# Performance work log

Hardware: AMD Instinct MI355X
Metric: run time of the kernel (lower is better)

## Reference

```python
import jax, jax.numpy as jnp
import numpy as np


def setup_inputs() -> dict:
    key = jax.random.key(0)
    ks = jax.random.split(key, 7)
    B, D, T, H = 32, 512, 4096, 512
    return {
        "query": jax.random.normal(ks[0], (B, D, 1), dtype=jnp.float32),
        "keys": jax.random.normal(ks[1], (B, D, T), dtype=jnp.float32),
        "values": jax.random.normal(ks[2], (B, D, T), dtype=jnp.float32),
        "w42": 0.01 * jax.random.normal(ks[3], (H, 2 * D), dtype=jnp.float32),
        "b4": 0.01 * jax.random.normal(ks[4], (H, 1), dtype=jnp.float32),
        "w54": 0.01 * jax.random.normal(ks[5], (1, H), dtype=jnp.float32),
        "b5": 0.01 * jax.random.normal(ks[6], (1, 1), dtype=jnp.float32),
    }


def reference(query, keys, values, w42, b4, w54, b5):
    D = keys.shape[1]
    # cat([keys, query.repeat T], dim=1) then w42 @ cat ==
    # w42[:, :D] @ keys + w42[:, D:] @ query (broadcast over T)
    n4 = (jnp.einsum('hd,bdt->bht', w42[:, :D], keys)
          + jnp.einsum('hd,bdo->bho', w42[:, D:], query)  # [B,H,1], broadcasts over T
          + b4)                                            # [H,1] broadcasts
    a4 = jnp.tanh(n4)                                      # [B,H,T]
    n5 = jnp.einsum('oh,bht->bot', w54, a4) + b5           # [B,1,T]
    # transpose(1,2) -> [B,T,1], softmax over dim=1 (T)
    a5 = jax.nn.softmax(n5[:, 0, :], axis=-1)              # [B,T]
    a6 = jnp.einsum('bvt,bt->bv', values, a5)[..., None]   # [B,Dv,1]
    return a6
```

## Files before the change

kernel.cpp:

```cpp
#include <hip/hip_runtime.h>
#include <hip/hip_bf16.h>
#include <cstdint>
#include <cstddef>

typedef __attribute__((ext_vector_type(4))) float f32x4;
typedef __attribute__((ext_vector_type(8))) short s16x8;
typedef __attribute__((ext_vector_type(4))) unsigned short u16x4;
typedef __attribute__((ext_vector_type(8))) unsigned short u16x8;

#define NB 32
#define DD 512
#define TT 4096
#define HH 512
#define TB 64
#define BK 32
#define NKK 16

__device__ __forceinline__ unsigned short f2bf(float f) {
  uint32_t u = __builtin_bit_cast(uint32_t, f);
  u += 0x7fffu + ((u >> 16) & 1u);
  return (unsigned short)(u >> 16);
}

__device__ __forceinline__ float tanh_fast(float x) {
  x = fminf(fmaxf(x, -15.f), 15.f);
  float e = __expf(2.f * x);
  return (e - 1.f) / (e + 1.f);
}

__global__ void kConvT(const float* __restrict__ w42, u16x8* __restrict__ W1swz) {
  int g = blockIdx.x * 256 + threadIdx.x;
  int h = g & 511, sk = g >> 9;
  int kk = sk >> 2, s = sk & 3;
  const float* src = &w42[h * 1024 + kk * 32 + s * 8];
  f32x4 v0 = *reinterpret_cast<const f32x4*>(src);
  f32x4 v1 = *reinterpret_cast<const f32x4*>(src + 4);
  u16x8 c;
  c[0] = f2bf(v0.x); c[1] = f2bf(v0.y); c[2] = f2bf(v0.z); c[3] = f2bf(v0.w);
  c[4] = f2bf(v1.x); c[5] = f2bf(v1.y); c[6] = f2bf(v1.z); c[7] = f2bf(v1.w);
  W1swz[kk * 2048 + s * 512 + h] = c;
}

__global__ void kQterm(const float* __restrict__ w42, const float* __restrict__ query,
                       const float* __restrict__ b4, float* __restrict__ qterm) {
  int wid = blockIdx.x * 4 + (threadIdx.x >> 6);
  int lane = threadIdx.x & 63;
  int b = wid >> 9, h = wid & 511;
  const float* wr = &w42[h * 1024 + 512];
  const float* q  = &query[b * 512];
  int d = lane * 8;
  f32x4 w0 = *(const f32x4*)&wr[d], w1 = *(const f32x4*)&wr[d + 4];
  f32x4 q0 = *(const f32x4*)&q[d],  q1 = *(const f32x4*)&q[d + 4];
  float s = w0.x*q0.x + w0.y*q0.y + w0.z*q0.z + w0.w*q0.w
          + w1.x*q1.x + w1.y*q1.y + w1.z*q1.z + w1.w*q1.w;
  #pragma unroll
  for (int off = 32; off; off >>= 1) s += __shfl_xor(s, off);
  if (lane == 0) qterm[b * 512 + h] = s + b4[h];
}

__global__ __launch_bounds__(256, 2) void kGemmE(
    const float* __restrict__ keys, const u16x8* __restrict__ W1swz,
    const float* __restrict__ qterm, const float* __restrict__ w54,
    float* __restrict__ e, float* __restrict__ Zp) {
  __shared__ s16x8 Bs[2 * 4 * 64];
  __shared__ float red[4][64];

  int bid = blockIdx.x;
  int b = bid >> 6, tblk = bid & 63;
  int t0 = tblk * TB;
  int tid = threadIdx.x, lane = tid & 63, w = tid >> 6;
  int lr = lane & 15, lg = lane >> 4;

  const float* kp = keys + (size_t)b * DD * TT + (size_t)(w * 8) * TT + t0 + lane;
  const s16x8* ap = reinterpret_cast<const s16x8*>(W1swz) + lg * 512 + w * 128 + lr;

  f32x4 acc[8][4];
  #pragma unroll
  for (int m = 0; m < 8; ++m)
    #pragma unroll
    for (int n = 0; n < 4; ++n) acc[m][n] = (f32x4){0.f, 0.f, 0.f, 0.f};

  s16x8 af[2][8];
  float r[2][8];
  #pragma unroll
  for (int m = 0; m < 8; ++m) af[0][m] = ap[m * 16];
  #pragma unroll
  for (int j = 0; j < 8; ++j) r[0][j] = kp[(size_t)j * TT];
  #pragma unroll
  for (int j = 0; j < 8; ++j) r[1][j] = kp[(size_t)(BK + j) * TT];

  #pragma unroll
  for (int kk = 0; kk < NKK; ++kk) {
    const int cur = kk & 1;
    s16x8 c;
    #pragma unroll
    for (int j = 0; j < 8; ++j) c[j] = (short)f2bf(r[cur][j]);
    Bs[(cur * 4 + w) * 64 + lane] = c;

    if (kk + 1 < NKK) {
      #pragma unroll
      for (int m = 0; m < 8; ++m) af[cur ^ 1][m] = ap[(kk + 1) * 2048 + m * 16];
    }
    if (kk + 2 < NKK) {
      const float* kp2 = kp + (size_t)(kk + 2) * BK * TT;
      #pragma unroll
      for (int j = 0; j < 8; ++j) r[cur][j] = kp2[(size_t)j * TT];
    }

    asm volatile("s_waitcnt lgkmcnt(0)" ::: "memory");
    __builtin_amdgcn_s_barrier();

    s16x8 bf[4];
    #pragma unroll
    for (int n = 0; n < 4; ++n)
      bf[n] = Bs[(cur * 4 + lg) * 64 + n * 16 + lr];

    #pragma unroll
    for (int m = 0; m < 8; ++m)
      #pragma unroll
      for (int n = 0; n < 4; ++n)
        acc[m][n] = __builtin_amdgcn_mfma_f32_16x16x32_bf16(af[cur][m], bf[n], acc[m][n], 0, 0, 0);
  }

  float part[4] = {0.f, 0.f, 0.f, 0.f};
  int hb = w * 128;
  #pragma unroll
  for (int m = 0; m < 8; ++m) {
    #pragma unroll
    for (int rr = 0; rr < 4; ++rr) {
      int h = hb + m * 16 + lg * 4 + rr;
      float qv = qterm[b * HH + h];
      float wv = w54[h];
      #pragma unroll
      for (int n = 0; n < 4; ++n)
        part[n] += wv * tanh_fast(acc[m][n][rr] + qv);
    }
  }
  #pragma unroll
  for (int n = 0; n < 4; ++n) {
    part[n] += __shfl_xor(part[n], 16);
    part[n] += __shfl_xor(part[n], 32);
  }
  if (lane < 16) {
    #pragma unroll
    for (int n = 0; n < 4; ++n) red[w][n * 16 + lane] = part[n];
  }
  __syncthreads();
  if (tid < 64) {
    float v = red[0][tid] + red[1][tid] + red[2][tid] + red[3][tid];
    float ev = __expf(v);
    e[b * TT + t0 + tid] = ev;
    float z = ev;
    #pragma unroll
    for (int off = 32; off; off >>= 1) z += __shfl_xor(z, off);
    if (tid == 0) Zp[b * 64 + tblk] = z;
  }
}

__global__ void kZinv(const float* __restrict__ Zp, float* __restrict__ Zinv) {
  int b = blockIdx.x, lane = threadIdx.x;
  float z = Zp[b * 64 + lane];
  #pragma unroll
  for (int off = 32; off; off >>= 1) z += __shfl_xor(z, off);
  if (lane == 0) Zinv[b] = 1.f / z;
}

__global__ void kOut(const float* __restrict__ values, const float* __restrict__ e,
                     const float* __restrict__ Zinv, float* __restrict__ out) {
  int blk = blockIdx.x;
  int b = blk >> 7;
  int wid = threadIdx.x >> 6, lane = threadIdx.x & 63;
  int v = (blk & 127) * 4 + wid;
  const float* row = &values[((size_t)b * 512 + v) * TT];
  const float* wv = &e[b * TT];
  float s = 0.f;
  #pragma unroll
  for (int i = 0; i < 16; ++i) {
    int t = (i * 64 + lane) * 4;
    f32x4 x = *(const f32x4*)&row[t];
    f32x4 y = *(const f32x4*)&wv[t];
    s += x.x * y.x + x.y * y.y + x.z * y.z + x.w * y.w;
  }
  #pragma unroll
  for (int off = 32; off; off >>= 1) s += __shfl_xor(s, off);
  if (lane == 0) out[b * 512 + v] = s * Zinv[b];
}

extern "C" void kernel_launch(void* const* d_in, const int* in_sizes, int n_in,
                              void* d_out, int out_size, void* d_ws, size_t ws_size,
                              hipStream_t stream) {
  const float* query  = (const float*)d_in[0];
  const float* keys   = (const float*)d_in[1];
  const float* values = (const float*)d_in[2];
  const float* w42    = (const float*)d_in[3];
  const float* b4     = (const float*)d_in[4];
  const float* w54    = (const float*)d_in[5];
  float* out = (float*)d_out;

  char* ws = (char*)d_ws;
  u16x8* W1swz = (u16x8*)ws;
  float* qterm = (float*)(ws + (512 << 10));
  float* Zp    = (float*)(ws + (576 << 10));
  float* Zinv  = (float*)(ws + (592 << 10));
  float* e     = (float*)(ws + (640 << 10));

  kConvT <<<128, 256, 0, stream>>>(w42, W1swz);
  kQterm <<<4096, 256, 0, stream>>>(w42, query, b4, qterm);
  kGemmE <<<2048, 256, 0, stream>>>(keys, W1swz, qterm, w54, e, Zp);
  kZinv  <<<32, 64, 0, stream>>>(Zp, Zinv);
  kOut   <<<4096, 256, 0, stream>>>(values, e, Zinv, out);
}
```

Before: 172.4 us.

## Retile GEMM over H quarters and 128-wide T tiles with swizzled LDS

The score GEMM now tiles each block over 128 hidden units and 128 time steps instead of all 512 hidden units by 64 steps. Blocks are remapped with a grid swizzle so the four H-quarter blocks for the same keys tile run close together and share keys in cache. Partial scores per H quarter go to a buffer, and a new softmax kernel sums them, exponentiates and computes the normalizer. Other changes: LDS XOR swizzling, packed bf16 conversion instructions, occupancy raised to 3, and nontemporal values loads with split accumulators in the output kernel. The cost is the extra partial-score traffic and keys re-reads across H blocks.

```diff
diff --git a/kernel.cpp b/kernel.cpp
--- a/kernel.cpp
+++ b/kernel.cpp
@@ -5,21 +5,24 @@
 
 typedef __attribute__((ext_vector_type(4))) float f32x4;
 typedef __attribute__((ext_vector_type(8))) short s16x8;
-typedef __attribute__((ext_vector_type(4))) unsigned short u16x4;
 typedef __attribute__((ext_vector_type(8))) unsigned short u16x8;
 
 #define NB 32
 #define DD 512
 #define TT 4096
 #define HH 512
-#define TB 64
-#define BK 32
 #define NKK 16
 
 __device__ __forceinline__ unsigned short f2bf(float f) {
   uint32_t u = __builtin_bit_cast(uint32_t, f);
   u += 0x7fffu + ((u >> 16) & 1u);
   return (unsigned short)(u >> 16);
+}
+
+__device__ __forceinline__ uint32_t cvtpk(float a, float b) {
+  uint32_t d;
+  asm("v_cvt_pk_bf16_f32 %0, %1, %2" : "=v"(d) : "v"(a), "v"(b));
+  return d;
 }
 
 __device__ __forceinline__ float tanh_fast(float x) {
@@ -58,53 +61,67 @@
   if (lane == 0) qterm[b * 512 + h] = s + b4[h];
 }
 
-__global__ __launch_bounds__(256, 2) void kGemmE(
+__global__ __launch_bounds__(256, 3) void kGemmE(
     const float* __restrict__ keys, const u16x8* __restrict__ W1swz,
     const float* __restrict__ qterm, const float* __restrict__ w54,
-    float* __restrict__ e, float* __restrict__ Zp) {
-  __shared__ s16x8 Bs[2 * 4 * 64];
-  __shared__ float red[4][64];
-
-  int bid = blockIdx.x;
-  int b = bid >> 6, tblk = bid & 63;
-  int t0 = tblk * TB;
-  int tid = threadIdx.x, lane = tid & 63, w = tid >> 6;
+    float* __restrict__ n5p) {
+  __shared__ s16x8 Bs[2][512];
+  __shared__ float red[2][128];
+
+  int p = blockIdx.x;
+  int lix = (p & 7) * 512 + (p >> 3);
+  int hq = lix & 3, tt = (lix >> 2) & 31, b = lix >> 7;
+  int h0 = hq * 128, t0 = tt * 128;
+
+  int tid = threadIdx.x, lane = tid & 63, wid = tid >> 6;
+  int wh = wid & 1, wt = wid >> 1;
   int lr = lane & 15, lg = lane >> 4;
 
-  const float* kp = keys + (size_t)b * DD * TT + (size_t)(w * 8) * TT + t0 + lane;
-  const s16x8* ap = reinterpret_cast<const s16x8*>(W1swz) + lg * 512 + w * 128 + lr;
-
-  f32x4 acc[8][4];
-  #pragma unroll
-  for (int m = 0; m < 8; ++m)
+  int s = tid >> 6, ta = tid & 63;
+  const float* kp = keys + (size_t)b * DD * TT + (size_t)(s * 8) * TT + t0 + ta;
+  int wiA = s * 128 + (ta ^ s), wiB = s * 128 + ((ta + 64) ^ s);
+  const s16x8* ap = reinterpret_cast<const s16x8*>(W1swz) + lg * 512 + h0 + wh * 64 + lr;
+  int rci[4];
+  #pragma unroll
+  for (int n = 0; n < 4; ++n) {
+    int t = wt * 64 + n * 16 + lr;
+    rci[n] = lg * 128 + (t ^ lg);
+  }
+
+  f32x4 acc[4][4];
+  #pragma unroll
+  for (int m = 0; m < 4; ++m)
     #pragma unroll
     for (int n = 0; n < 4; ++n) acc[m][n] = (f32x4){0.f, 0.f, 0.f, 0.f};
 
-  s16x8 af[2][8];
-  float r[2][8];
-  #pragma unroll
-  for (int m = 0; m < 8; ++m) af[0][m] = ap[m * 16];
-  #pragma unroll
-  for (int j = 0; j < 8; ++j) r[0][j] = kp[(size_t)j * TT];
-  #pragma unroll
-  for (int j = 0; j < 8; ++j) r[1][j] = kp[(size_t)(BK + j) * TT];
+  float r[16];
+  #pragma unroll
+  for (int j = 0; j < 8; ++j) r[j] = kp[(size_t)j * TT];
+  #pragma unroll
+  for (int j = 0; j < 8; ++j) r[8 + j] = kp[(size_t)j * TT + 64];
 
   #pragma unroll
   for (int kk = 0; kk < NKK; ++kk) {
     const int cur = kk & 1;
-    s16x8 c;
-    #pragma unroll
-    for (int j = 0; j < 8; ++j) c[j] = (short)f2bf(r[cur][j]);
-    Bs[(cur * 4 + w) * 64 + lane] = c;
+    s16x8 af[4];
+    #pragma unroll
+    for (int m = 0; m < 4; ++m) af[m] = ap[kk * 2048 + m * 16];
+
+    union { uint32_t u[4]; s16x8 v; } ca, cb;
+    #pragma unroll
+    for (int j = 0; j < 4; ++j) {
+      ca.u[j] = cvtpk(r[2 * j], r[2 * j + 1]);
+      cb.u[j] = cvtpk(r[8 + 2 * j], r[9 + 2 * j]);
+    }
+    Bs[cur][wiA] = ca.v;
+    Bs[cur][wiB] = cb.v;
 
     if (kk + 1 < NKK) {
-      #pragma unroll
-      for (int m = 0; m < 8; ++m) af[cur ^ 1][m] = ap[(kk + 1) * 2048 + m * 16];
-    }
-    if (kk + 2 < NKK) {
-      const float* kp2 = kp + (size_t)(kk + 2) * BK * TT;
-      #pragma unroll
-      for (int j = 0; j < 8; ++j) r[cur][j] = kp2[(size_t)j * TT];
+      const float* kp2 = kp + (size_t)(kk + 1) * 32 * TT;
+      #pragma unroll
+      for (int j = 0; j < 8; ++j) r[j] = kp2[(size_t)j * TT];
+      #pragma unroll
+      for (int j = 0; j < 8; ++j) r[8 + j] = kp2[(size_t)j * TT + 64];
     }
 
     asm volatile("s_waitcnt lgkmcnt(0)" ::: "memory");
@@ -112,28 +129,26 @@
 
     s16x8 bf[4];
     #pragma unroll
-    for (int n = 0; n < 4; ++n)
-      bf[n] = Bs[(cur * 4 + lg) * 64 + n * 16 + lr];
-
-    #pragma unroll
-    for (int m = 0; m < 8; ++m)
+    for (int n = 0; n < 4; ++n) bf[n] = Bs[cur][rci[n]];
+
+    #pragma unroll
+    for (int m = 0; m < 4; ++m)
       #pragma unroll
       for (int n = 0; n < 4; ++n)
-        acc[m][n] = __builtin_amdgcn_mfma_f32_16x16x32_bf16(af[cur][m], bf[n], acc[m][n], 0, 0, 0);
+        acc[m][n] = __builtin_amdgcn_mfma_f32_16x16x32_bf16(af[m], bf[n], acc[m][n], 0, 0, 0);
   }
 
   float part[4] = {0.f, 0.f, 0.f, 0.f};
-  int hb = w * 128;
-  #pragma unroll
-  for (int m = 0; m < 8; ++m) {
+  #pragma unroll
+  for (int m = 0; m < 4; ++m) {
     #pragma unroll
     for (int rr = 0; rr < 4; ++rr) {
-      int h = hb + m * 16 + lg * 4 + rr;
+      int h = h0 + wh * 64 + m * 16 + lg * 4 + rr;
       float qv = qterm[b * HH + h];
-      float wv = w54[h];
+      float wvv = w54[h];
       #pragma unroll
       for (int n = 0; n < 4; ++n)
-        part[n] += wv * tanh_fast(acc[m][n][rr] + qv);
+        part[n] += wvv * tanh_fast(acc[m][n][rr] + qv);
     }
   }
   #pragma unroll
@@ -143,26 +158,35 @@
   }
   if (lane < 16) {
     #pragma unroll
-    for (int n = 0; n < 4; ++n) red[w][n * 16 + lane] = part[n];
+    for (int n = 0; n < 4; ++n) red[wh][wt * 64 + n * 16 + lane] = part[n];
   }
   __syncthreads();
-  if (tid < 64) {
-    float v = red[0][tid] + red[1][tid] + red[2][tid] + red[3][tid];
+  if (tid < 128) {
+    float v = red[0][tid] + red[1][tid];
+    n5p[((size_t)hq * NB + b) * TT + t0 + tid] = v;
+  }
+}
+
+__global__ void kSoftE(const float* __restrict__ n5p, float* __restrict__ e,
+                       float* __restrict__ Zinv) {
+  int b = blockIdx.x, tid = threadIdx.x;
+  int lane = tid & 63, wid = tid >> 6;
+  __shared__ float zsh[4];
+  float z = 0.f;
+  #pragma unroll
+  for (int i = 0; i < 16; ++i) {
+    int t = tid + i * 256;
+    float v = n5p[(0 * NB + b) * TT + t] + n5p[(1 * NB + b) * TT + t]
+            + n5p[(2 * NB + b) * TT + t] + n5p[(3 * NB + b) * TT + t];
     float ev = __expf(v);
-    e[b * TT + t0 + tid] = ev;
-    float z = ev;
-    #pragma unroll
-    for (int off = 32; off; off >>= 1) z += __shfl_xor(z, off);
-    if (tid == 0) Zp[b * 64 + tblk] = z;
-  }
-}
-
-__global__ void kZinv(const float* __restrict__ Zp, float* __restrict__ Zinv) {
-  int b = blockIdx.x, lane = threadIdx.x;
-  float z = Zp[b * 64 + lane];
+    e[b * TT + t] = ev;
+    z += ev;
+  }
   #pragma unroll
   for (int off = 32; off; off >>= 1) z += __shfl_xor(z, off);
-  if (lane == 0) Zinv[b] = 1.f / z;
+  if (lane == 0) zsh[wid] = z;
+  __syncthreads();
+  if (tid == 0) Zinv[b] = 1.f / (zsh[0] + zsh[1] + zsh[2] + zsh[3]);
 }
 
 __global__ void kOut(const float* __restrict__ values, const float* __restrict__ e,
@@ -173,14 +197,17 @@
   int v = (blk & 127) * 4 + wid;
   const float* row = &values[((size_t)b * 512 + v) * TT];
   const float* wv = &e[b * TT];
-  float s = 0.f;
+  float s0 = 0.f, s1 = 0.f, s2 = 0.f, s3 = 0.f;
   #pragma unroll
   for (int i = 0; i < 16; ++i) {
     int t = (i * 64 + lane) * 4;
-    f32x4 x = *(const f32x4*)&row[t];
+    f32x4 x = __builtin_nontemporal_load(reinterpret_cast<const f32x4*>(&row[t]));
     f32x4 y = *(const f32x4*)&wv[t];
-    s += x.x * y.x + x.y * y.y + x.z * y.z + x.w * y.w;
-  }
+    float d = x.x * y.x + x.y * y.y + x.z * y.z + x.w * y.w;
+    if ((i & 3) == 0) s0 += d; else if ((i & 3) == 1) s1 += d;
+    else if ((i & 3) == 2) s2 += d; else s3 += d;
+  }
+  float s = (s0 + s1) + (s2 + s3);
   #pragma unroll
   for (int off = 32; off; off >>= 1) s += __shfl_xor(s, off);
   if (lane == 0) out[b * 512 + v] = s * Zinv[b];
@@ -200,13 +227,13 @@
   char* ws = (char*)d_ws;
   u16x8* W1swz = (u16x8*)ws;
   float* qterm = (float*)(ws + (512 << 10));
-  float* Zp    = (float*)(ws + (576 << 10));
-  float* Zinv  = (float*)(ws + (592 << 10));
+  float* Zinv  = (float*)(ws + (576 << 10));
   float* e     = (float*)(ws + (640 << 10));
+  float* n5p   = (float*)(ws + (1152 << 10));
 
   kConvT <<<128, 256, 0, stream>>>(w42, W1swz);
   kQterm <<<4096, 256, 0, stream>>>(w42, query, b4, qterm);
-  kGemmE <<<2048, 256, 0, stream>>>(keys, W1swz, qterm, w54, e, Zp);
-  kZinv  <<<32, 64, 0, stream>>>(Zp, Zinv);
+  kGemmE <<<4096, 256, 0, stream>>>(keys, W1swz, qterm, w54, n5p);
+  kSoftE <<<32, 256, 0, stream>>>(n5p, e, Zinv);
   kOut   <<<4096, 256, 0, stream>>>(values, e, Zinv, out);
 }
```

Result: slower. 184.0 us (+6.7%).

## Load keys directly into MFMA B-fragments, drop LDS staging and barrier

Applied to the files above, without the earlier changes.

The GEMM kernel no longer stages bf16-converted keys through shared memory with a per-iteration barrier. Each wave now loads the key elements it needs for its own B fragments straight from global memory and converts them with the packed v_cvt_pk_bf16_f32 instruction. This removes LDS traffic and synchronisation, but every wave now re-reads the same keys tile (4x redundant global/L2 loads), uncoalesced in 16-wide strips, and prefetch depth drops from two steps to one. The output kernel also uses nontemporal loads for values and four independent accumulators.

```diff
diff --git a/kernel.cpp b/kernel.cpp
--- a/kernel.cpp
+++ b/kernel.cpp
@@ -5,21 +5,24 @@
 
 typedef __attribute__((ext_vector_type(4))) float f32x4;
 typedef __attribute__((ext_vector_type(8))) short s16x8;
-typedef __attribute__((ext_vector_type(4))) unsigned short u16x4;
 typedef __attribute__((ext_vector_type(8))) unsigned short u16x8;
 
 #define NB 32
 #define DD 512
 #define TT 4096
 #define HH 512
-#define TB 64
-#define BK 32
 #define NKK 16
 
 __device__ __forceinline__ unsigned short f2bf(float f) {
   uint32_t u = __builtin_bit_cast(uint32_t, f);
   u += 0x7fffu + ((u >> 16) & 1u);
   return (unsigned short)(u >> 16);
+}
+
+__device__ __forceinline__ uint32_t cvtpk(float a, float b) {
+  uint32_t d;
+  asm("v_cvt_pk_bf16_f32 %0, %1, %2" : "=v"(d) : "v"(a), "v"(b));
+  return d;
 }
 
 __device__ __forceinline__ float tanh_fast(float x) {
@@ -62,16 +65,15 @@
     const float* __restrict__ keys, const u16x8* __restrict__ W1swz,
     const float* __restrict__ qterm, const float* __restrict__ w54,
     float* __restrict__ e, float* __restrict__ Zp) {
-  __shared__ s16x8 Bs[2 * 4 * 64];
   __shared__ float red[4][64];
 
   int bid = blockIdx.x;
   int b = bid >> 6, tblk = bid & 63;
-  int t0 = tblk * TB;
+  int t0 = tblk * 64;
   int tid = threadIdx.x, lane = tid & 63, w = tid >> 6;
   int lr = lane & 15, lg = lane >> 4;
 
-  const float* kp = keys + (size_t)b * DD * TT + (size_t)(w * 8) * TT + t0 + lane;
+  const float* kb = keys + (size_t)b * DD * TT + (size_t)(lg * 8) * TT + t0 + lr;
   const s16x8* ap = reinterpret_cast<const s16x8*>(W1swz) + lg * 512 + w * 128 + lr;
 
   f32x4 acc[8][4];
@@ -81,40 +83,35 @@
     for (int n = 0; n < 4; ++n) acc[m][n] = (f32x4){0.f, 0.f, 0.f, 0.f};
 
   s16x8 af[2][8];
-  float r[2][8];
+  float rb[4][8];
   #pragma unroll
   for (int m = 0; m < 8; ++m) af[0][m] = ap[m * 16];
   #pragma unroll
-  for (int j = 0; j < 8; ++j) r[0][j] = kp[(size_t)j * TT];
-  #pragma unroll
-  for (int j = 0; j < 8; ++j) r[1][j] = kp[(size_t)(BK + j) * TT];
+  for (int n = 0; n < 4; ++n)
+    #pragma unroll
+    for (int j = 0; j < 8; ++j) rb[n][j] = kb[(size_t)j * TT + n * 16];
 
   #pragma unroll
   for (int kk = 0; kk < NKK; ++kk) {
     const int cur = kk & 1;
-    s16x8 c;
-    #pragma unroll
-    for (int j = 0; j < 8; ++j) c[j] = (short)f2bf(r[cur][j]);
-    Bs[(cur * 4 + w) * 64 + lane] = c;
-
+    s16x8 bf[4];
+    #pragma unroll
+    for (int n = 0; n < 4; ++n) {
+      union { uint32_t u[4]; s16x8 v; } c;
+      #pragma unroll
+      for (int jj = 0; jj < 4; ++jj)
+        c.u[jj] = cvtpk(rb[n][2 * jj], rb[n][2 * jj + 1]);
+      bf[n] = c.v;
+    }
     if (kk + 1 < NKK) {
       #pragma unroll
       for (int m = 0; m < 8; ++m) af[cur ^ 1][m] = ap[(kk + 1) * 2048 + m * 16];
+      const float* kb2 = kb + (size_t)(kk + 1) * 32 * TT;
+      #pragma unroll
+      for (int n = 0; n < 4; ++n)
+        #pragma unroll
+        for (int j = 0; j < 8; ++j) rb[n][j] = kb2[(size_t)j * TT + n * 16];
     }
-    if (kk + 2 < NKK) {
-      const float* kp2 = kp + (size_t)(kk + 2) * BK * TT;
-      #pragma unroll
-      for (int j = 0; j < 8; ++j) r[cur][j] = kp2[(size_t)j * TT];
-    }
-
-    asm volatile("s_waitcnt lgkmcnt(0)" ::: "memory");
-    __builtin_amdgcn_s_barrier();
-
-    s16x8 bf[4];
-    #pragma unroll
-    for (int n = 0; n < 4; ++n)
-      bf[n] = Bs[(cur * 4 + lg) * 64 + n * 16 + lr];
-
     #pragma unroll
     for (int m = 0; m < 8; ++m)
       #pragma unroll
@@ -173,14 +170,17 @@
   int v = (blk & 127) * 4 + wid;
   const float* row = &values[((size_t)b * 512 + v) * TT];
   const float* wv = &e[b * TT];
-  float s = 0.f;
+  float s0 = 0.f, s1 = 0.f, s2 = 0.f, s3 = 0.f;
   #pragma unroll
   for (int i = 0; i < 16; ++i) {
     int t = (i * 64 + lane) * 4;
-    f32x4 x = *(const f32x4*)&row[t];
+    f32x4 x = __builtin_nontemporal_load(reinterpret_cast<const f32x4*>(&row[t]));
     f32x4 y = *(const f32x4*)&wv[t];
-    s += x.x * y.x + x.y * y.y + x.z * y.z + x.w * y.w;
-  }
+    float d = x.x * y.x + x.y * y.y + x.z * y.z + x.w * y.w;
+    if ((i & 3) == 0) s0 += d; else if ((i & 3) == 1) s1 += d;
+    else if ((i & 3) == 2) s2 += d; else s3 += d;
+  }
+  float s = (s0 + s1) + (s2 + s3);
   #pragma unroll
   for (int off = 32; off; off >>= 1) s += __shfl_xor(s, off);
   if (lane == 0) out[b * 512 + v] = s * Zinv[b];
```

New measurement: 190.2 us. 1.1x slower.
